# Performance work log

Measured on AMD Instinct MI355X. Metric: run time of the kernel, lower is better.

The kernel has to match this reference:

```python
import jax, jax.numpy as jnp
import numpy as np


def _make_kernels():
    # 4 fixed 3x3x3 stencils: identity + Sobel x/y/z (separable smooth x smooth x derivative)
    d = np.array([-1.0, 0.0, 1.0], dtype=np.float32)
    s = np.array([1.0, 2.0, 1.0], dtype=np.float32)
    sx = np.einsum('i,j,k->ijk', s, s, d) / 16.0
    sy = np.einsum('i,j,k->ijk', s, d, s) / 16.0
    sz = np.einsum('i,j,k->ijk', d, s, s) / 16.0
    ident = np.zeros((3, 3, 3), dtype=np.float32)
    ident[1, 1, 1] = 1.0
    return np.stack([ident, sx, sy, sz], axis=0)  # (4,3,3,3)


def setup_inputs() -> dict:
    key = jax.random.key(0)
    x = jax.random.normal(key, (4, 16, 64, 64, 64), dtype=jnp.float32)
    kernels = jnp.asarray(_make_kernels())  # fixed buffer, (4,3,3,3)
    return {"x": x, "kernels": kernels}


def reference(x, kernels):
    B, C, D, H, W = x.shape
    # replicate padding by 1 on each spatial side
    xp = jnp.pad(x, ((0, 0), (0, 0), (1, 1), (1, 1), (1, 1)), mode='edge')
    # depthwise: every channel gets all 4 filters -> fold channels into batch,
    # run one conv with 4 output channels, then restore torch's [k*C + c] ordering
    xr = xp.reshape(B * C, 1, D + 2, H + 2, W + 2)
    k = kernels[:, None]  # (4,1,3,3,3), OIDHW
    out = jax.lax.conv_general_dilated(
        xr, k, window_strides=(1, 1, 1), padding='VALID',
        dimension_numbers=('NCDHW', 'OIDHW', 'NCDHW'))  # (B*C,4,D,H,W)
    out = out.reshape(B, C, 4, D, H, W).transpose(0, 2, 1, 3, 4, 5)
    return out.reshape(B, 4 * C, D, H, W)
```

## Files before the change

kernel.cpp:

```cpp
#include <hip/hip_runtime.h>


#define B_ 4
#define C_ 16
#define D_ 64
#define H_ 64
#define W_ 64

typedef float float4v __attribute__((ext_vector_type(4)));

__global__ __launch_bounds__(256) void perceive3d_kernel(
    const float* __restrict__ x, float* __restrict__ out)
{
    const int lane = threadIdx.x;
    const int quad = lane & 15;
    const int hsub = lane >> 4;
    const int h    = blockIdx.x * 16 + threadIdx.y * 4 + hsub;
    const int d    = blockIdx.y;
    const int bc   = blockIdx.z;
    const int b    = bc >> 4;
    const int c    = bc & 15;

    const float* xb = x + (size_t)bc * (D_ * H_ * W_);

    const int dm = (d == 0) ? 0 : d - 1;
    const int dp = (d == D_ - 1) ? D_ - 1 : d + 1;
    const int hm = (h == 0) ? 0 : h - 1;
    const int hp = (h == H_ - 1) ? H_ - 1 : h + 1;

    const int dzo[3] = { dm * (H_ * W_), d * (H_ * W_), dp * (H_ * W_) };
    const int hyo[3] = { hm * W_,        h * W_,        hp * W_ };
    const float si[3] = { 1.0f, 2.0f, 1.0f };

    float4v sx = {0,0,0,0}, sy = {0,0,0,0}, sz = {0,0,0,0};
    float4v center = {0,0,0,0};

#pragma unroll
    for (int i = 0; i < 3; ++i) {
#pragma unroll
        for (int j = 0; j < 3; ++j) {
            const float* row = xb + dzo[i] + hyo[j];
            float4v q = *(const float4v*)(row + 4 * quad);

            float left  = __shfl_up(q.w, 1);
            float right = __shfl_down(q.x, 1);
            if (quad == 0)      left  = q.x;
            if (quad == 15)     right = q.w;

            float4v am = { left, q.x, q.y, q.z };
            float4v ap = { q.y, q.z, q.w, right };

            float4v sw = am + 2.0f * q + ap;
            float4v dw = ap - am;

            const float cij = si[i] * si[j];
            sx += cij * dw;
            if (j == 0)      sy -= si[i] * sw;
            else if (j == 2) sy += si[i] * sw;
            if (i == 0)      sz -= si[j] * sw;
            else if (i == 2) sz += si[j] * sw;
            if (i == 1 && j == 1) center = q;
        }
    }

    sx *= (1.0f / 16.0f);
    sy *= (1.0f / 16.0f);
    sz *= (1.0f / 16.0f);

    const size_t dhw     = (size_t)D_ * H_ * W_;
    const size_t cdhw    = (size_t)C_ * dhw;
    const size_t spatial = ((size_t)d * H_ + h) * W_ + 4 * quad;

    float* o = out + ((size_t)(b * 4) * C_ + c) * dhw + spatial;
    __builtin_nontemporal_store(center, (float4v*)(o + 0 * cdhw));
    __builtin_nontemporal_store(sx,     (float4v*)(o + 1 * cdhw));
    __builtin_nontemporal_store(sy,     (float4v*)(o + 2 * cdhw));
    __builtin_nontemporal_store(sz,     (float4v*)(o + 3 * cdhw));
}

extern "C" void kernel_launch(void* const* d_in, const int* in_sizes, int n_in,
                              void* d_out, int out_size, void* d_ws, size_t ws_size,
                              hipStream_t stream) {
    (void)in_sizes; (void)n_in; (void)d_ws; (void)ws_size; (void)out_size;
    const float* x = (const float*)d_in[0];
    float* out = (float*)d_out;

    dim3 block(64, 4, 1);
    dim3 grid(H_ / 16, D_, B_ * C_);
    perceive3d_kernel<<<grid, block, 0, stream>>>(x, out);
}
```

Before: 315.3 us.

## Stream depth planes per thread with rolling window of separable partial sums

```diff
diff --git a/kernel.cpp b/kernel.cpp
--- a/kernel.cpp
+++ b/kernel.cpp
@@ -6,8 +6,40 @@
 #define D_ 64
 #define H_ 64
 #define W_ 64
+#define DCHUNK 8
 
 typedef float float4v __attribute__((ext_vector_type(4)));
+
+struct PQR { float4v P, Q, R, qc; };
+
+__device__ __forceinline__ PQR load_plane(const float* __restrict__ xb,
+                                          int z, int hm, int h, int hp,
+                                          int quad)
+{
+    const float* pl = xb + z * (H_ * W_);
+    const int rows[3] = { hm, h, hp };
+    float4v qmid = {0,0,0,0};
+    float4v sw[3], dw[3];
+#pragma unroll
+    for (int r = 0; r < 3; ++r) {
+        float4v v = *(const float4v*)(pl + rows[r] * W_ + 4 * quad);
+        float left  = __shfl_up(v.w, 1);
+        float right = __shfl_down(v.x, 1);
+        if (quad == 0)  left  = v.x;
+        if (quad == 15) right = v.w;
+        float4v am = { left, v.x, v.y, v.z };
+        float4v ap = { v.y, v.z, v.w, right };
+        sw[r] = am + 2.0f * v + ap;
+        dw[r] = ap - am;
+        if (r == 1) qmid = v;
+    }
+    PQR o;
+    o.P  = dw[0] + 2.0f * dw[1] + dw[2];
+    o.Q  = sw[2] - sw[0];
+    o.R  = sw[0] + 2.0f * sw[1] + sw[2];
+    o.qc = qmid;
+    return o;
+}
 
 __global__ __launch_bounds__(256) void perceive3d_kernel(
     const float* __restrict__ x, float* __restrict__ out)
@@ -16,66 +48,45 @@
     const int quad = lane & 15;
     const int hsub = lane >> 4;
     const int h    = blockIdx.x * 16 + threadIdx.y * 4 + hsub;
-    const int d    = blockIdx.y;
+    const int d0   = blockIdx.y * DCHUNK;
     const int bc   = blockIdx.z;
     const int b    = bc >> 4;
     const int c    = bc & 15;
 
-    const float* xb = x + (size_t)bc * (D_ * H_ * W_);
-
-    const int dm = (d == 0) ? 0 : d - 1;
-    const int dp = (d == D_ - 1) ? D_ - 1 : d + 1;
     const int hm = (h == 0) ? 0 : h - 1;
     const int hp = (h == H_ - 1) ? H_ - 1 : h + 1;
 
-    const int dzo[3] = { dm * (H_ * W_), d * (H_ * W_), dp * (H_ * W_) };
-    const int hyo[3] = { hm * W_,        h * W_,        hp * W_ };
-    const float si[3] = { 1.0f, 2.0f, 1.0f };
+    const float* xb = x + (size_t)bc * (D_ * H_ * W_);
 
-    float4v sx = {0,0,0,0}, sy = {0,0,0,0}, sz = {0,0,0,0};
-    float4v center = {0,0,0,0};
+    PQR s[3];
+    s[0] = load_plane(xb, (d0 == 0) ? 0 : d0 - 1, hm, h, hp, quad);
+    s[1] = load_plane(xb, d0, hm, h, hp, quad);
+
+    const size_t dhw  = (size_t)D_ * H_ * W_;
+    const size_t cdhw = (size_t)C_ * dhw;
+    float* o = out + ((size_t)(b * 4) * C_ + c) * dhw
+                   + ((size_t)d0 * H_ + h) * W_ + 4 * quad;
 
 #pragma unroll
-    for (int i = 0; i < 3; ++i) {
-#pragma unroll
-        for (int j = 0; j < 3; ++j) {
-            const float* row = xb + dzo[i] + hyo[j];
-            float4v q = *(const float4v*)(row + 4 * quad);
+    for (int t = 0; t < DCHUNK; ++t) {
+        int zn = d0 + t + 1;
+        if (zn > D_ - 1) zn = D_ - 1;
+        s[(t + 2) % 3] = load_plane(xb, zn, hm, h, hp, quad);
 
-            float left  = __shfl_up(q.w, 1);
-            float right = __shfl_down(q.x, 1);
-            if (quad == 0)      left  = q.x;
-            if (quad == 15)     right = q.w;
+        const PQR& a = s[t % 3];
+        const PQR& m = s[(t + 1) % 3];
+        const PQR& p = s[(t + 2) % 3];
 
-            float4v am = { left, q.x, q.y, q.z };
-            float4v ap = { q.y, q.z, q.w, right };
+        float4v sx = (a.P + 2.0f * m.P + p.P) * (1.0f / 16.0f);
+        float4v sy = (a.Q + 2.0f * m.Q + p.Q) * (1.0f / 16.0f);
+        float4v sz = (p.R - a.R) * (1.0f / 16.0f);
 
-            float4v sw = am + 2.0f * q + ap;
-            float4v dw = ap - am;
-
-            const float cij = si[i] * si[j];
-            sx += cij * dw;
-            if (j == 0)      sy -= si[i] * sw;
-            else if (j == 2) sy += si[i] * sw;
-            if (i == 0)      sz -= si[j] * sw;
-            else if (i == 2) sz += si[j] * sw;
-            if (i == 1 && j == 1) center = q;
-        }
+        float* od = o + (size_t)t * (H_ * W_);
+        __builtin_nontemporal_store(m.qc, (float4v*)(od + 0 * cdhw));
+        __builtin_nontemporal_store(sx,   (float4v*)(od + 1 * cdhw));
+        __builtin_nontemporal_store(sy,   (float4v*)(od + 2 * cdhw));
+        __builtin_nontemporal_store(sz,   (float4v*)(od + 3 * cdhw));
     }
-
-    sx *= (1.0f / 16.0f);
-    sy *= (1.0f / 16.0f);
-    sz *= (1.0f / 16.0f);
-
-    const size_t dhw     = (size_t)D_ * H_ * W_;
-    const size_t cdhw    = (size_t)C_ * dhw;
-    const size_t spatial = ((size_t)d * H_ + h) * W_ + 4 * quad;
-
-    float* o = out + ((size_t)(b * 4) * C_ + c) * dhw + spatial;
-    __builtin_nontemporal_store(center, (float4v*)(o + 0 * cdhw));
-    __builtin_nontemporal_store(sx,     (float4v*)(o + 1 * cdhw));
-    __builtin_nontemporal_store(sy,     (float4v*)(o + 2 * cdhw));
-    __builtin_nontemporal_store(sz,     (float4v*)(o + 3 * cdhw));
 }
 
 extern "C" void kernel_launch(void* const* d_in, const int* in_sizes, int n_in,
@@ -86,6 +97,6 @@
     float* out = (float*)d_out;
 
     dim3 block(64, 4, 1);
-    dim3 grid(H_ / 16, D_, B_ * C_);
+    dim3 grid(H_ / 16, D_ / DCHUNK, B_ * C_);
     perceive3d_kernel<<<grid, block, 0, stream>>>(x, out);
 }
```

Measured after the change: 316.8 us. No clear change (+0.5%).
